# Optimization experiments

Hardware: AMD Instinct MI355X
Metric: run time of the kernel (lower is better)

Reference implementation:

```python
import jax, jax.numpy as jnp
import numpy as np

N = 4096     # nagents
OBS = 256    # obs_size
HID = 256    # hid_size
G = 64       # gat_hid_size
H1 = 4       # gat_num_heads (so H1*G == HID)
H2 = 1       # gat_num_heads_out
A = 64       # actions
QMAX = 255.0  # 2**quant_bits - 1, quant_min = 0
NEG_SLOPE = 0.2


def _lstm_cell(x, h, c, Wih, Whh, bih, bhh):
    gates = x @ Wih.T + bih + h @ Whh.T + bhh
    i, f, g, o = jnp.split(gates, 4, axis=-1)
    c2 = jax.nn.sigmoid(f) * c + jax.nn.sigmoid(i) * jnp.tanh(g)
    h2 = jax.nn.sigmoid(o) * jnp.tanh(c2)
    return h2, c2


def _gat(x, adj, W, a_i, a_j, b, average, self_loop_type):
    # x: [n, in], adj: [n, n], W: [in, H*g], a_i/a_j: [H, g], b: [H*g] or [g_out]
    n = x.shape[0]
    H, g = a_i.shape
    eye = jnp.eye(n, dtype=adj.dtype)
    if self_loop_type == 1:      # force self-loops
        adj = adj * (1.0 - eye) + eye
    elif self_loop_type == 2:    # remove self-loops
        adj = adj * (1.0 - eye)
    h = (x @ W).reshape(n, H, g)                      # [n, H, g]
    ci = jnp.einsum('nhg,hg->hn', h, a_i)             # [H, n]
    cj = jnp.einsum('nhg,hg->hn', h, a_j)             # [H, n]
    e = jax.nn.leaky_relu(ci[:, :, None] + cj[:, None, :], NEG_SLOPE)  # [H, n, n]
    att = jax.nn.softmax(jnp.where(adj[None] > 0, e, -9e15), axis=-1) * adj[None]
    out = jnp.einsum('hij,jhg->ihg', att, h)          # [n, H, g]
    out = out.mean(axis=1) if average else out.reshape(n, H * g)
    return out + b


def _fake_quant(t, bmask):
    # dynamic-range fake quantization over masked entries (min/max detached)
    big = jnp.asarray(1e30, t.dtype)
    mn = jax.lax.stop_gradient(jnp.min(jnp.where(bmask, t, big)))
    mx = jax.lax.stop_gradient(jnp.max(jnp.where(bmask, t, -big)))
    eq = mn == mx
    mn = jnp.where(eq, mn - 0.01, mn)
    mx = jnp.where(eq, mx + 0.01, mx)
    scale = (mx - mn) / QMAX
    zp = jnp.round(-mn / scale)  # quant_min = 0
    deq = (jnp.clip(jnp.round(t / scale + zp), 0.0, QMAX) - zp) * scale
    return jnp.where(bmask, deq, t)


def _qloss(t, bmask):
    return jnp.sum(jnp.where(bmask, jnp.log2(2.0 * QMAX * jnp.abs(t) + 1.0), 0.0))


def _forward(obs, h0, c0, Wobs, bobs, Wih, Whh, bih, bhh,
             W1, ai1, aj1, b1, W2, ai2, aj2, b2, Wv, bv, Wa, ba):
    n = N
    mask = jnp.ones((n, 1), obs.dtype)        # all agents alive
    enc = obs.reshape(n, -1) @ Wobs + bobs    # obs encoder, squeeze batch=1
    h, c = _lstm_cell(enc, h0, c0, Wih, Whh, bih, bhh)
    comm = h
    bmask = jnp.broadcast_to(mask > 0, comm.shape)
    comm = _fake_quant(comm, bmask)
    loss = _qloss(comm, bmask)
    comm = comm * mask
    adj = jnp.ones((n, n), obs.dtype) * mask * mask.T   # complete graph
    comm = _gat(comm, adj, W1, ai1, aj1, b1, average=False, self_loop_type=1)
    comm = jax.nn.elu(comm)
    bmask2 = jnp.broadcast_to(mask > 0, comm.shape)
    comm = _fake_quant(comm, bmask2)
    loss = loss + _qloss(comm, bmask2)
    comm = _gat(comm, adj, W2, ai2, aj2, b2, average=True, self_loop_type=1)
    comm = comm * mask
    value = jnp.concatenate([h, comm], axis=-1) @ Wv + bv              # [n, 1]
    feat = jnp.concatenate([h.reshape(1, n, -1), comm.reshape(1, n, -1)], axis=-1)
    logp = jax.nn.log_softmax(feat @ Wa + ba, axis=-1)                 # [1, n, A]
    return logp, value, h, c, loss


def setup_inputs() -> dict:
    key = jax.random.key(0)
    ks = jax.random.split(key, 21)
    def rn(k, shape, sc=0.05):
        return jax.random.normal(k, shape, dtype=jnp.float32) * sc
    return {
        'obs': rn(ks[0], (1, N, OBS), 1.0),
        'h0': rn(ks[1], (N, HID), 1.0),
        'c0': rn(ks[2], (N, HID), 1.0),
        'Wobs': rn(ks[3], (OBS, HID)),
        'bobs': rn(ks[4], (HID,)),
        'Wih': rn(ks[5], (4 * HID, HID)),
        'Whh': rn(ks[6], (4 * HID, HID)),
        'bih': rn(ks[7], (4 * HID,)),
        'bhh': rn(ks[8], (4 * HID,)),
        'W1': rn(ks[9], (HID, H1 * G)),
        'ai1': rn(ks[10], (H1, G)),
        'aj1': rn(ks[11], (H1, G)),
        'b1': rn(ks[12], (H1 * G,)),
        'W2': rn(ks[13], (H1 * G, H2 * HID)),
        'ai2': rn(ks[14], (H2, HID)),
        'aj2': rn(ks[15], (H2, HID)),
        'b2': rn(ks[16], (HID,)),
        'Wv': rn(ks[17], (2 * HID, 1)),
        'bv': rn(ks[18], (1,)),
        'Wa': rn(ks[19], (2 * HID, A)),
        'ba': rn(ks[20], (A,)),
    }


def reference(obs, h0, c0, Wobs, bobs, Wih, Whh, bih, bhh,
              W1, ai1, aj1, b1, W2, ai2, aj2, b2, Wv, bv, Wa, ba):
    return _forward(obs, h0, c0, Wobs, bobs, Wih, Whh, bih, bhh,
                    W1, ai1, aj1, b1, W2, ai2, aj2, b2, Wv, bv, Wa, ba)
```

## Files before the change

### kernel.cpp

```cpp
#include <hip/hip_runtime.h>
#include <math.h>

typedef __attribute__((ext_vector_type(8))) short short8;
typedef __attribute__((ext_vector_type(4))) float floatx4;

__device__ __forceinline__ ushort f2b(float f) {
  unsigned u = __float_as_uint(f);
  unsigned r = u + 0x7FFFu + ((u >> 16) & 1u);
  return (ushort)(r >> 16);
}

__global__ __launch_bounds__(256) void prep_kernel(
    const float* __restrict__ obs, ushort* __restrict__ obs_bf,
    const float* __restrict__ h0, ushort* __restrict__ h0_bf,
    const float* __restrict__ Wih, ushort* __restrict__ Wih_bf,
    const float* __restrict__ Whh, ushort* __restrict__ Whh_bf,
    const float* __restrict__ Wobs, ushort* __restrict__ WobsT,
    const float* __restrict__ W1, ushort* __restrict__ W1T,
    const float* __restrict__ W2, ushort* __restrict__ W2T,
    const float* __restrict__ Wa, const float* __restrict__ Wv,
    const float* __restrict__ ba, const float* __restrict__ bv,
    const float* __restrict__ bih, const float* __restrict__ bhh,
    ushort* __restrict__ WaTe, float* __restrict__ bias_ext, float* __restrict__ bias12)
{
  __shared__ float tile[32][33];
  const int bid = blockIdx.x;
  const int tid = threadIdx.x;
  if (bid < 1024) {
    const int q0 = 262144, q1 = 262144, q2 = 65536, q3 = 65536;
    const int tot = q0 + q1 + q2 + q3;
    for (int idx = bid * 256 + tid; idx < tot; idx += 1024 * 256) {
      const float* s; ushort* d; int i = idx;
      if (i < q0) { s = obs; d = obs_bf; }
      else if ((i -= q0) < q1) { s = h0; d = h0_bf; }
      else if ((i -= q1) < q2) { s = Wih; d = Wih_bf; }
      else { i -= q2; s = Whh; d = Whh_bf; }
      const float4 v = *(const float4*)(s + (size_t)i * 4);
      ushort4 o; o.x = f2b(v.x); o.y = f2b(v.y); o.z = f2b(v.z); o.w = f2b(v.w);
      *(ushort4*)(d + (size_t)i * 4) = o;
    }
  } else if (bid < 1216) {
    const int t = bid - 1024;
    const int mat = t >> 6, sub = t & 63;
    const float* in = mat == 0 ? Wobs : (mat == 1 ? W1 : W2);
    ushort* outp = mat == 0 ? WobsT : (mat == 1 ? W1T : W2T);
    const int c0 = (sub & 7) * 32, r0 = (sub >> 3) * 32;
    const int tx = tid & 31, ty = tid >> 5;
    #pragma unroll
    for (int p = 0; p < 32; p += 8)
      tile[ty + p][tx] = in[(size_t)(r0 + ty + p) * 256 + c0 + tx];
    __syncthreads();
    #pragma unroll
    for (int p = 0; p < 32; p += 8)
      outp[(size_t)(c0 + ty + p) * 256 + r0 + tx] = f2b(tile[tx][ty + p]);
  } else {
    const int idx = (bid - 1216) * 256 + tid;
    if (idx < 65536) {
      const int n = idx >> 9, k = idx & 511;
      const float v = n < 64 ? Wa[(size_t)k * 64 + n] : (n == 64 ? Wv[k] : 0.0f);
      WaTe[idx] = f2b(v);
    } else if (idx < 65536 + 128) {
      const int n = idx - 65536;
      bias_ext[n] = n < 64 ? ba[n] : (n == 64 ? bv[0] : 0.0f);
    } else if (idx < 65536 + 128 + 1024) {
      const int n = idx - 65536 - 128;
      bias12[n] = bih[n] + bhh[n];
    }
  }
}

template<int BM, int BN, bool OUT_BF16>
__global__ __launch_bounds__(256) void mfma_gemm(
    const ushort* __restrict__ A1, int lda1,
    const ushort* __restrict__ B1, int ldb1, int K1,
    const ushort* __restrict__ A2, int lda2,
    const ushort* __restrict__ B2, int ldb2, int K2,
    const float* __restrict__ bias,
    void* __restrict__ Cv, int N)
{
  constexpr int LDT = 40;
  __shared__ __align__(16) ushort As[BM * LDT];
  __shared__ __align__(16) ushort Bs[BN * LDT];
  const int tid = threadIdx.x;
  const int wave = tid >> 6, lane = tid & 63;
  const int wr = wave >> 1, wc = wave & 1;
  const int m0 = blockIdx.y * BM, n0 = blockIdx.x * BN;
  constexpr int MI = BM / 32;
  constexpr int NI = BN / 32;
  floatx4 acc[MI][NI] = {};
  const int r = tid >> 2, kq = tid & 3;
  const int lm = lane & 15, lq = lane >> 4;
  const int Ktot = K1 + K2;
  for (int k0 = 0; k0 < Ktot; k0 += 32) {
    const ushort* A; const ushort* B; int lda, ldb, kk;
    if (k0 < K1) { A = A1; B = B1; lda = lda1; ldb = ldb1; kk = k0; }
    else         { A = A2; B = B2; lda = lda2; ldb = ldb2; kk = k0 - K1; }
    #pragma unroll
    for (int p = 0; p < BM / 64; ++p) {
      const int rr = r + p * 64;
      *(float4*)&As[rr * LDT + kq * 8] =
          *(const float4*)&A[(size_t)(m0 + rr) * lda + kk + kq * 8];
    }
    #pragma unroll
    for (int p = 0; p < BN / 64; ++p) {
      const int rr = r + p * 64;
      *(float4*)&Bs[rr * LDT + kq * 8] =
          *(const float4*)&B[(size_t)(n0 + rr) * ldb + kk + kq * 8];
    }
    __syncthreads();
    short8 af[MI], bfr[NI];
    #pragma unroll
    for (int i = 0; i < MI; ++i)
      af[i] = *(const short8*)&As[(wr * (BM / 2) + i * 16 + lm) * LDT + lq * 8];
    #pragma unroll
    for (int j = 0; j < NI; ++j)
      bfr[j] = *(const short8*)&Bs[(wc * (BN / 2) + j * 16 + lm) * LDT + lq * 8];
    #pragma unroll
    for (int i = 0; i < MI; ++i)
      #pragma unroll
      for (int j = 0; j < NI; ++j)
        acc[i][j] = __builtin_amdgcn_mfma_f32_16x16x32_bf16(af[i], bfr[j], acc[i][j], 0, 0, 0);
    __syncthreads();
  }
  #pragma unroll
  for (int i = 0; i < MI; ++i) {
    #pragma unroll
    for (int j = 0; j < NI; ++j) {
      const int col = n0 + wc * (BN / 2) + j * 16 + lm;
      const float badd = bias ? bias[col] : 0.0f;
      #pragma unroll
      for (int t = 0; t < 4; ++t) {
        const int row = m0 + wr * (BM / 2) + i * 16 + lq * 4 + t;
        const float v = acc[i][j][t] + badd;
        if (OUT_BF16) ((ushort*)Cv)[(size_t)row * N + col] = f2b(v);
        else          ((float*)Cv)[(size_t)row * N + col] = v;
      }
    }
  }
}

__global__ __launch_bounds__(256) void lstm_elem_kernel(
    const float* __restrict__ gates, const float* __restrict__ c0,
    float* __restrict__ h_out, float* __restrict__ c_out, ushort* __restrict__ h_bf,
    float* __restrict__ pmn, float* __restrict__ pmx)
{
  const int i = blockIdx.x, d = threadIdx.x;
  const float* g = gates + (size_t)i * 1024;
  const float xi = g[d], xf = g[256 + d], xg = g[512 + d], xo = g[768 + d];
  const float c = c0[(size_t)i * 256 + d];
  const float si = 1.0f / (1.0f + expf(-xi));
  const float sf = 1.0f / (1.0f + expf(-xf));
  const float so = 1.0f / (1.0f + expf(-xo));
  const float c2 = sf * c + si * tanhf(xg);
  const float h2 = so * tanhf(c2);
  h_out[(size_t)i * 256 + d] = h2;
  c_out[(size_t)i * 256 + d] = c2;
  h_bf[(size_t)i * 256 + d] = f2b(h2);
  float mn = h2, mx = h2;
  #pragma unroll
  for (int o = 32; o > 0; o >>= 1) {
    mn = fminf(mn, __shfl_xor(mn, o));
    mx = fmaxf(mx, __shfl_xor(mx, o));
  }
  __shared__ float smn[4], smx[4];
  if ((d & 63) == 0) { smn[d >> 6] = mn; smx[d >> 6] = mx; }
  __syncthreads();
  if (d == 0) {
    pmn[i] = fminf(fminf(smn[0], smn[1]), fminf(smn[2], smn[3]));
    pmx[i] = fmaxf(fmaxf(smx[0], smx[1]), fmaxf(smx[2], smx[3]));
  }
}

__global__ __launch_bounds__(256) void quant_kernel(
    const float4* __restrict__ x, ushort* __restrict__ q, int n4,
    const float* __restrict__ pmn, const float* __restrict__ pmx, int np,
    float* __restrict__ part)
{
  __shared__ float smn[4], smx[4], sl[4], bmn, bmx;
  float mn = 3.0e38f, mx = -3.0e38f;
  for (int i = threadIdx.x; i < np; i += 256) {
    mn = fminf(mn, pmn[i]); mx = fmaxf(mx, pmx[i]);
  }
  #pragma unroll
  for (int o = 32; o > 0; o >>= 1) {
    mn = fminf(mn, __shfl_xor(mn, o));
    mx = fmaxf(mx, __shfl_xor(mx, o));
  }
  if ((threadIdx.x & 63) == 0) { smn[threadIdx.x >> 6] = mn; smx[threadIdx.x >> 6] = mx; }
  __syncthreads();
  if (threadIdx.x == 0) {
    bmn = fminf(fminf(smn[0], smn[1]), fminf(smn[2], smn[3]));
    bmx = fmaxf(fmaxf(smx[0], smx[1]), fmaxf(smx[2], smx[3]));
  }
  __syncthreads();
  mn = bmn; mx = bmx;
  if (mn == mx) { mn -= 0.01f; mx += 0.01f; }
  const float scale = (mx - mn) / 255.0f;
  const float zp = rintf(-mn / scale);
  float lsum = 0.0f;
  for (int idx = blockIdx.x * 256 + threadIdx.x; idx < n4; idx += gridDim.x * 256) {
    const float4 t = x[idx];
    float d0, d1, d2, d3;
    { float qq = fminf(fmaxf(rintf(t.x / scale + zp), 0.0f), 255.0f);
      d0 = (qq - zp) * scale; lsum += log2f(510.0f * fabsf(d0) + 1.0f); }
    { float qq = fminf(fmaxf(rintf(t.y / scale + zp), 0.0f), 255.0f);
      d1 = (qq - zp) * scale; lsum += log2f(510.0f * fabsf(d1) + 1.0f); }
    { float qq = fminf(fmaxf(rintf(t.z / scale + zp), 0.0f), 255.0f);
      d2 = (qq - zp) * scale; lsum += log2f(510.0f * fabsf(d2) + 1.0f); }
    { float qq = fminf(fmaxf(rintf(t.w / scale + zp), 0.0f), 255.0f);
      d3 = (qq - zp) * scale; lsum += log2f(510.0f * fabsf(d3) + 1.0f); }
    ushort4 o; o.x = f2b(d0); o.y = f2b(d1); o.z = f2b(d2); o.w = f2b(d3);
    *(ushort4*)(q + (size_t)idx * 4) = o;
  }
  #pragma unroll
  for (int o = 32; o > 0; o >>= 1) lsum += __shfl_xor(lsum, o);
  if ((threadIdx.x & 63) == 0) sl[threadIdx.x >> 6] = lsum;
  __syncthreads();
  if (threadIdx.x == 0) part[blockIdx.x] = sl[0] + sl[1] + sl[2] + sl[3];
}

__global__ __launch_bounds__(256) void cicj1_kernel(
    const float* __restrict__ h1, const float* __restrict__ ai, const float* __restrict__ aj,
    float* __restrict__ ci, float* __restrict__ cj)
{
  const int w = threadIdx.x >> 6, lane = threadIdx.x & 63;
  const int i = blockIdx.x * 4 + w;
  #pragma unroll
  for (int hd = 0; hd < 4; ++hd) {
    const float v = h1[(size_t)i * 256 + hd * 64 + lane];
    float pi = v * ai[hd * 64 + lane];
    float pj = v * aj[hd * 64 + lane];
    #pragma unroll
    for (int o = 32; o > 0; o >>= 1) { pi += __shfl_xor(pi, o); pj += __shfl_xor(pj, o); }
    if (lane == 0) { ci[hd * 4096 + i] = pi; cj[hd * 4096 + i] = pj; }
  }
}

__global__ __launch_bounds__(256) void cicj2_kernel(
    const float* __restrict__ h2, const float* __restrict__ ai, const float* __restrict__ aj,
    float* __restrict__ ci, float* __restrict__ cj)
{
  const int w = threadIdx.x >> 6, lane = threadIdx.x & 63;
  const int i = blockIdx.x * 4 + w;
  float pi = 0.f, pj = 0.f;
  #pragma unroll
  for (int r = 0; r < 4; ++r) {
    const float v = h2[(size_t)i * 256 + r * 64 + lane];
    pi += v * ai[r * 64 + lane];
    pj += v * aj[r * 64 + lane];
  }
  #pragma unroll
  for (int o = 32; o > 0; o >>= 1) { pi += __shfl_xor(pi, o); pj += __shfl_xor(pj, o); }
  if (lane == 0) { ci[i] = pi; cj[i] = pj; }
}

__global__ __launch_bounds__(1024) void rank_sort_kernel(
    const float* __restrict__ c, float* __restrict__ sc, int* __restrict__ pm)
{
  __shared__ float lc[4096];
  __shared__ int scnt[16][64];
  const int head = blockIdx.x >> 6;
  const int seg = blockIdx.x & 63;
  const float* ch = c + head * 4096;
  for (int idx = threadIdx.x; idx < 4096; idx += 1024) lc[idx] = ch[idx];
  __syncthreads();
  const int jl = threadIdx.x & 63;
  const int kg = threadIdx.x >> 6;
  const int j = seg * 64 + jl;
  const float my = lc[j];
  int cnt = 0;
  const int k0 = kg * 256;
  #pragma unroll 8
  for (int k = k0; k < k0 + 256; ++k) {
    const float ck = lc[k];
    cnt += (ck < my || (ck == my && k < j)) ? 1 : 0;
  }
  scnt[kg][jl] = cnt;
  __syncthreads();
  if (threadIdx.x < 64) {
    int rank = 0;
    #pragma unroll
    for (int g = 0; g < 16; ++g) rank += scnt[g][threadIdx.x];
    const int jj = seg * 64 + threadIdx.x;
    sc[head * 4096 + rank] = lc[jj];
    pm[head * 4096 + rank] = jj;
  }
}

__global__ __launch_bounds__(128) void local_scan1(
    const float* __restrict__ h1, const float* __restrict__ sc, const int* __restrict__ pm,
    float* __restrict__ PUl, float* __restrict__ PVl,
    float* __restrict__ dUl, float* __restrict__ dVl,
    float* __restrict__ cku, float* __restrict__ ckv,
    float* __restrict__ ckus, float* __restrict__ ckvs)
{
  const int head = blockIdx.x >> 6;
  const int chunk = blockIdx.x & 63;
  const int wave = threadIdx.x >> 6;
  const int lane = threadIdx.x & 63;
  const float cmax = sc[head * 4096 + 4095];
  const int base = head * 4096 + chunk * 64;
  const float cv = sc[base + lane];
  const float u = expf(cv - cmax);
  const float v = expf(0.2f * (cv - cmax));
  const int myj = pm[base + lane];
  const float* hrow = h1 + head * 64 + lane;
  if (wave == 0) {
    float iu = u, iv = v;
    #pragma unroll
    for (int o = 1; o < 64; o <<= 1) {
      const float tu = __shfl_up(iu, o), tv = __shfl_up(iv, o);
      if (lane >= o) { iu += tu; iv += tv; }
    }
    const float totU = __shfl(iu, 63), totV = __shfl(iv, 63);
    dVl[base + lane] = iv - v;
    dUl[base + lane] = totU - (iu - u);
    if (lane == 0) { ckus[head * 64 + chunk] = totU; ckvs[head * 64 + chunk] = totV; }
    float accV = 0.f;
    #pragma unroll 16
    for (int k = 0; k < 64; ++k) {
      const float vk = __shfl(v, k);
      const int j = __shfl(myj, k);
      PVl[(size_t)(base + k) * 64 + lane] = accV;
      accV += vk * hrow[(size_t)j * 256];
    }
    ckv[(head * 64 + chunk) * 64 + lane] = accV;
  } else {
    float accU = 0.f;
    #pragma unroll 16
    for (int k = 63; k >= 0; --k) {
      const float uk = __shfl(u, k);
      const int j = __shfl(myj, k);
      accU += uk * hrow[(size_t)j * 256];
      PUl[(size_t)(base + k) * 64 + lane] = accU;
    }
    cku[(head * 64 + chunk) * 64 + lane] = accU;
  }
}

__global__ __launch_bounds__(256) void local_scan2(
    const float* __restrict__ h2, const float* __restrict__ sc, const int* __restrict__ pm,
    float* __restrict__ PUl, float* __restrict__ PVl,
    float* __restrict__ dUl, float* __restrict__ dVl,
    float* __restrict__ cku, float* __restrict__ ckv,
    float* __restrict__ ckus, float* __restrict__ ckvs)
{
  __shared__ float su[64], sv[64];
  __shared__ int sj[64];
  const int chunk = blockIdx.y;
  const int colgrp = blockIdx.x;
  const int tid = threadIdx.x;
  const int wave = tid >> 6, lane = tid & 63;
  const float cmax = sc[4095];
  const int base = chunk * 64;
  if (tid < 64) {
    const float cv = sc[base + tid];
    const float u = expf(cv - cmax);
    const float v = expf(0.2f * (cv - cmax));
    su[tid] = u; sv[tid] = v; sj[tid] = pm[base + tid];
    if (colgrp == 0) {
      float iu = u, iv = v;
      #pragma unroll
      for (int o = 1; o < 64; o <<= 1) {
        const float tu = __shfl_up(iu, o), tv = __shfl_up(iv, o);
        if (lane >= o) { iu += tu; iv += tv; }
      }
      const float totU = __shfl(iu, 63), totV = __shfl(iv, 63);
      dVl[base + lane] = iv - v;
      dUl[base + lane] = totU - (iu - u);
      if (lane == 0) { ckus[chunk] = totU; ckvs[chunk] = totV; }
    }
  }
  __syncthreads();
  const int col = colgrp * 128 + (wave & 1) * 64 + lane;
  if (wave < 2) {
    float accV = 0.f;
    #pragma unroll 16
    for (int k = 0; k < 64; ++k) {
      PVl[(size_t)(base + k) * 256 + col] = accV;
      accV += sv[k] * h2[(size_t)sj[k] * 256 + col];
    }
    ckv[chunk * 256 + col] = accV;
  } else {
    float accU = 0.f;
    #pragma unroll 16
    for (int k = 63; k >= 0; --k) {
      accU += su[k] * h2[(size_t)sj[k] * 256 + col];
      PUl[(size_t)(base + k) * 256 + col] = accU;
    }
    cku[chunk * 256 + col] = accU;
  }
}

__global__ __launch_bounds__(64) void prefix1_kernel(
    const float* __restrict__ cku, const float* __restrict__ ckv,
    const float* __restrict__ ckus, const float* __restrict__ ckvs,
    float* __restrict__ sufU, float* __restrict__ prefV,
    float* __restrict__ sufUs, float* __restrict__ prefVs)
{
  const int head = blockIdx.x, lane = threadIdx.x;
  float acc = 0.f;
  for (int c = 0; c < 64; ++c) {
    prefV[(head * 65 + c) * 64 + lane] = acc;
    acc += ckv[(head * 64 + c) * 64 + lane];
  }
  prefV[(head * 65 + 64) * 64 + lane] = acc;
  acc = 0.f;
  sufU[(head * 65 + 64) * 64 + lane] = 0.f;
  for (int c = 63; c >= 0; --c) {
    acc += cku[(head * 64 + c) * 64 + lane];
    sufU[(head * 65 + c) * 64 + lane] = acc;
  }
  {
    const float vs = ckvs[head * 64 + lane];
    const float us = ckus[head * 64 + lane];
    float iv = vs, iu = us;
    #pragma unroll
    for (int o = 1; o < 64; o <<= 1) {
      const float tv = __shfl_up(iv, o), tu = __shfl_up(iu, o);
      if (lane >= o) { iv += tv; iu += tu; }
    }
    prefVs[head * 65 + lane] = iv - vs;
    const float totU = __shfl(iu, 63);
    sufUs[head * 65 + lane] = totU - iu + us;
    if (lane == 63) {
      prefVs[head * 65 + 64] = iv;
      sufUs[head * 65 + 64] = 0.f;
    }
  }
}

__global__ __launch_bounds__(256) void prefix2_kernel(
    const float* __restrict__ cku, const float* __restrict__ ckv,
    const float* __restrict__ ckus, const float* __restrict__ ckvs,
    float* __restrict__ sufU, float* __restrict__ prefV,
    float* __restrict__ sufUs, float* __restrict__ prefVs)
{
  const int col = threadIdx.x;
  const int lane = col & 63;
  float acc = 0.f;
  for (int c = 0; c < 64; ++c) {
    prefV[c * 256 + col] = acc;
    acc += ckv[c * 256 + col];
  }
  prefV[64 * 256 + col] = acc;
  acc = 0.f;
  sufU[64 * 256 + col] = 0.f;
  for (int c = 63; c >= 0; --c) {
    acc += cku[c * 256 + col];
    sufU[c * 256 + col] = acc;
  }
  if (col < 64) {
    const float vs = ckvs[lane];
    const float us = ckus[lane];
    float iv = vs, iu = us;
    #pragma unroll
    for (int o = 1; o < 64; o <<= 1) {
      const float tv = __shfl_up(iv, o), tu = __shfl_up(iu, o);
      if (lane >= o) { iv += tv; iu += tu; }
    }
    prefVs[lane] = iv - vs;
    const float totU = __shfl(iu, 63);
    sufUs[lane] = totU - iu + us;
    if (lane == 63) { prefVs[64] = iv; sufUs[64] = 0.f; }
  }
}

__global__ __launch_bounds__(256) void combine1_kernel(
    const float* __restrict__ ci, const float* __restrict__ sc,
    const float* __restrict__ sufU, const float* __restrict__ prefV,
    const float* __restrict__ sufUs, const float* __restrict__ prefVs,
    const float* __restrict__ PUl, const float* __restrict__ PVl,
    const float* __restrict__ dUl, const float* __restrict__ dVl,
    const float* __restrict__ b1, float* __restrict__ out,
    float* __restrict__ pmn, float* __restrict__ pmx)
{
  const int i = blockIdx.x;
  const int head = threadIdx.x >> 6;
  const int lane = threadIdx.x & 63;
  const float* sch = sc + head * 4096;
  const float civ = ci[head * 4096 + i];
  const float cmax = sch[4095];
  const float sarg = civ + cmax;
  const float m = sarg > 0.f ? sarg : 0.2f * sarg;
  const float Af = expf(sarg - m);
  const float Bf = expf(0.2f * sarg - m);
  const float t = -civ;
  int lo = 0, hi = 4096;
  while (lo < hi) {
    const int mid = (lo + hi) >> 1;
    if (sch[mid] > t) hi = mid; else lo = mid + 1;
  }
  const int s = lo;
  float accP, accN, dP, dN;
  if (s == 4096) {
    accP = 0.f; dP = 0.f;
    accN = prefV[(head * 65 + 64) * 64 + lane];
    dN = prefVs[head * 65 + 64];
  } else {
    const int cs = s >> 6;
    accP = sufU[(head * 65 + cs + 1) * 64 + lane] + PUl[(size_t)(head * 4096 + s) * 64 + lane];
    accN = prefV[(head * 65 + cs) * 64 + lane] + PVl[(size_t)(head * 4096 + s) * 64 + lane];
    dP = sufUs[head * 65 + cs + 1] + dUl[head * 4096 + s];
    dN = prefVs[head * 65 + cs] + dVl[head * 4096 + s];
  }
  const float num = Af * accP + Bf * accN;
  const float den = Af * dP + Bf * dN;
  const float o = num / den + b1[head * 64 + lane];
  const float oe = o > 0.f ? o : expm1f(o);
  out[(size_t)i * 256 + head * 64 + lane] = oe;
  float mn = oe, mx = oe;
  #pragma unroll
  for (int of = 32; of > 0; of >>= 1) {
    mn = fminf(mn, __shfl_xor(mn, of));
    mx = fmaxf(mx, __shfl_xor(mx, of));
  }
  __shared__ float smn[4], smx[4];
  if (lane == 0) { smn[head] = mn; smx[head] = mx; }
  __syncthreads();
  if (threadIdx.x == 0) {
    pmn[i] = fminf(fminf(smn[0], smn[1]), fminf(smn[2], smn[3]));
    pmx[i] = fmaxf(fmaxf(smx[0], smx[1]), fmaxf(smx[2], smx[3]));
  }
}

__global__ __launch_bounds__(256) void combine2_kernel(
    const float* __restrict__ ci, const float* __restrict__ sc,
    const float* __restrict__ sufU, const float* __restrict__ prefV,
    const float* __restrict__ sufUs, const float* __restrict__ prefVs,
    const float* __restrict__ PUl, const float* __restrict__ PVl,
    const float* __restrict__ dUl, const float* __restrict__ dVl,
    const float* __restrict__ b2, ushort* __restrict__ outb)
{
  const int i = blockIdx.x;
  const int col = threadIdx.x;
  const float civ = ci[i];
  const float cmax = sc[4095];
  const float sarg = civ + cmax;
  const float m = sarg > 0.f ? sarg : 0.2f * sarg;
  const float Af = expf(sarg - m);
  const float Bf = expf(0.2f * sarg - m);
  const float t = -civ;
  int lo = 0, hi = 4096;
  while (lo < hi) {
    const int mid = (lo + hi) >> 1;
    if (sc[mid] > t) hi = mid; else lo = mid + 1;
  }
  const int s = lo;
  float accP, accN, dP, dN;
  if (s == 4096) {
    accP = 0.f; dP = 0.f;
    accN = prefV[64 * 256 + col];
    dN = prefVs[64];
  } else {
    const int cs = s >> 6;
    accP = sufU[(cs + 1) * 256 + col] + PUl[(size_t)s * 256 + col];
    accN = prefV[cs * 256 + col] + PVl[(size_t)s * 256 + col];
    dP = sufUs[cs + 1] + dUl[s];
    dN = prefVs[cs] + dVl[s];
  }
  const float num = Af * accP + Bf * accN;
  const float den = Af * dP + Bf * dN;
  outb[(size_t)i * 256 + col] = f2b(num / den + b2[col]);
}

__global__ __launch_bounds__(64) void logsoftmax_kernel(
    const float* __restrict__ logits_ext, float* __restrict__ out,
    float* __restrict__ out_value,
    const float* __restrict__ p1, const float* __restrict__ p2,
    float* __restrict__ out_loss)
{
  const int i = blockIdx.x, lane = threadIdx.x;
  if (i == 4096) {
    float s = 0.f;
    #pragma unroll
    for (int k = 0; k < 4; ++k) s += p1[lane + k * 64] + p2[lane + k * 64];
    #pragma unroll
    for (int o = 32; o > 0; o >>= 1) s += __shfl_xor(s, o);
    if (lane == 0) out_loss[0] = s;
    return;
  }
  const float x = logits_ext[(size_t)i * 128 + lane];
  float mx = x;
  #pragma unroll
  for (int o = 32; o > 0; o >>= 1) mx = fmaxf(mx, __shfl_xor(mx, o));
  float e = expf(x - mx);
  #pragma unroll
  for (int o = 32; o > 0; o >>= 1) e += __shfl_xor(e, o);
  out[(size_t)i * 64 + lane] = x - mx - logf(e);
  if (lane == 0) out_value[i] = logits_ext[(size_t)i * 128 + 64];
}

extern "C" void kernel_launch(void* const* d_in, const int* in_sizes, int n_in,
                              void* d_out, int out_size, void* d_ws, size_t ws_size,
                              hipStream_t stream) {
  const float* obs  = (const float*)d_in[0];
  const float* h0   = (const float*)d_in[1];
  const float* c0   = (const float*)d_in[2];
  const float* Wobs = (const float*)d_in[3];
  const float* bobs = (const float*)d_in[4];
  const float* Wih  = (const float*)d_in[5];
  const float* Whh  = (const float*)d_in[6];
  const float* bih  = (const float*)d_in[7];
  const float* bhh  = (const float*)d_in[8];
  const float* W1   = (const float*)d_in[9];
  const float* ai1  = (const float*)d_in[10];
  const float* aj1  = (const float*)d_in[11];
  const float* b1   = (const float*)d_in[12];
  const float* W2   = (const float*)d_in[13];
  const float* ai2  = (const float*)d_in[14];
  const float* aj2  = (const float*)d_in[15];
  const float* b2   = (const float*)d_in[16];
  const float* Wv   = (const float*)d_in[17];
  const float* bv   = (const float*)d_in[18];
  const float* Wa   = (const float*)d_in[19];
  const float* ba   = (const float*)d_in[20];

  float* out       = (float*)d_out;
  float* out_logp  = out;
  float* out_value = out + 262144;
  float* out_h     = out + 266240;
  float* out_c     = out + 1314816;
  float* out_loss  = out + 2363392;

  char* ws = (char*)d_ws;
  float* part1  = (float*)(ws + 256);
  float* part2  = (float*)(ws + 1280);
  float* pmn    = (float*)(ws + 2304);
  float* pmx    = (float*)(ws + 18688);
  const size_t MB = 1048576;
  const size_t base = 35072;
  ushort* obs_bf  = (ushort*)(ws + base);
  ushort* h0_bf   = (ushort*)(ws + base + 2 * MB);
  ushort* Wih_bf  = (ushort*)(ws + base + 4 * MB);
  ushort* Whh_bf  = (ushort*)(ws + base + 4 * MB + 524288);
  ushort* WobsT   = (ushort*)(ws + base + 5 * MB);
  ushort* W1T     = (ushort*)(ws + base + 5 * MB + 131072);
  ushort* W2T     = (ushort*)(ws + base + 5 * MB + 262144);
  ushort* WaTe    = (ushort*)(ws + base + 5 * MB + 393216);
  float*  bias_ext= (float*) (ws + base + 5 * MB + 524288);
  float*  bias12  = (float*) (ws + base + 5 * MB + 525312);
  ushort* enc_bf  = (ushort*)(ws + base + 6 * MB);
  ushort* h_bf    = (ushort*)(ws + base + 8 * MB);
  ushort* comm_q1 = (ushort*)(ws + base + 10 * MB);
  ushort* comm_q2 = (ushort*)(ws + base + 12 * MB);
  ushort* comm2_bf= (ushort*)(ws + base + 14 * MB);
  float*  gates   = (float*) (ws + base + 16 * MB);
  float*  h1      = gates;
  float*  comm1e  = (float*)((char*)gates + 4 * MB);
  float*  h2b     = (float*)((char*)gates + 8 * MB);
  float*  logits  = (float*)((char*)gates + 12 * MB);
  size_t so = base + 32 * MB;
  auto alloc = [&](size_t bytes) { size_t r = so; so += (bytes + 255) & ~255ull; return (char*)ws + r; };
  float* ci1    = (float*)alloc(4 * 4096 * 4);
  float* cj1    = (float*)alloc(4 * 4096 * 4);
  float* sc1    = (float*)alloc(4 * 4096 * 4);
  int*   pm1    = (int*)  alloc(4 * 4096 * 4);
  float* cku1   = (float*)alloc(4 * 64 * 64 * 4);
  float* ckv1   = (float*)alloc(4 * 64 * 64 * 4);
  float* ckus1  = (float*)alloc(4 * 64 * 4);
  float* ckvs1  = (float*)alloc(4 * 64 * 4);
  float* sufU1  = (float*)alloc(4 * 65 * 64 * 4);
  float* prefV1 = (float*)alloc(4 * 65 * 64 * 4);
  float* sufUs1 = (float*)alloc(4 * 65 * 4);
  float* prefVs1= (float*)alloc(4 * 65 * 4);
  float* ci2    = (float*)alloc(4096 * 4);
  float* cj2    = (float*)alloc(4096 * 4);
  float* sc2    = (float*)alloc(4096 * 4);
  int*   pm2    = (int*)  alloc(4096 * 4);
  float* cku2   = (float*)alloc(64 * 256 * 4);
  float* ckv2   = (float*)alloc(64 * 256 * 4);
  float* ckus2  = (float*)alloc(64 * 4);
  float* ckvs2  = (float*)alloc(64 * 4);
  float* sufU2  = (float*)alloc(65 * 256 * 4);
  float* prefV2 = (float*)alloc(65 * 256 * 4);
  float* sufUs2 = (float*)alloc(65 * 4);
  float* prefVs2= (float*)alloc(65 * 4);
  float* PUl    = (float*)alloc(4 * 4096 * 64 * 4);
  float* PVl    = (float*)alloc(4 * 4096 * 64 * 4);
  float* dUl    = (float*)alloc(4 * 4096 * 4);
  float* dVl    = (float*)alloc(4 * 4096 * 4);

  const dim3 b256(256);
  const int N4 = 262144;

  prep_kernel<<<dim3(1477), b256, 0, stream>>>(
      obs, obs_bf, h0, h0_bf, Wih, Wih_bf, Whh, Whh_bf,
      Wobs, WobsT, W1, W1T, W2, W2T,
      Wa, Wv, ba, bv, bih, bhh, WaTe, bias_ext, bias12);
  mfma_gemm<64, 64, true><<<dim3(4, 64), b256, 0, stream>>>(
      obs_bf, 256, WobsT, 256, 256, nullptr, 0, nullptr, 0, 0, bobs, enc_bf, 256);
  mfma_gemm<128, 128, false><<<dim3(8, 32), b256, 0, stream>>>(
      enc_bf, 256, Wih_bf, 256, 256, h0_bf, 256, Whh_bf, 256, 256, bias12, gates, 1024);
  lstm_elem_kernel<<<dim3(4096), b256, 0, stream>>>(gates, c0, out_h, out_c, h_bf, pmn, pmx);
  quant_kernel<<<dim3(256), b256, 0, stream>>>(
      (const float4*)out_h, comm_q1, N4, pmn, pmx, 4096, part1);
  mfma_gemm<64, 64, false><<<dim3(4, 64), b256, 0, stream>>>(
      comm_q1, 256, W1T, 256, 256, nullptr, 0, nullptr, 0, 0, nullptr, h1, 256);
  cicj1_kernel<<<dim3(1024), b256, 0, stream>>>(h1, ai1, aj1, ci1, cj1);
  rank_sort_kernel<<<dim3(256), dim3(1024), 0, stream>>>(cj1, sc1, pm1);
  local_scan1<<<dim3(256), dim3(128), 0, stream>>>(h1, sc1, pm1,
      PUl, PVl, dUl, dVl, cku1, ckv1, ckus1, ckvs1);
  prefix1_kernel<<<dim3(4), dim3(64), 0, stream>>>(cku1, ckv1, ckus1, ckvs1,
                                                   sufU1, prefV1, sufUs1, prefVs1);
  combine1_kernel<<<dim3(4096), b256, 0, stream>>>(ci1, sc1,
      sufU1, prefV1, sufUs1, prefVs1, PUl, PVl, dUl, dVl, b1, comm1e, pmn, pmx);
  quant_kernel<<<dim3(256), b256, 0, stream>>>(
      (const float4*)comm1e, comm_q2, N4, pmn, pmx, 4096, part2);
  mfma_gemm<64, 64, false><<<dim3(4, 64), b256, 0, stream>>>(
      comm_q2, 256, W2T, 256, 256, nullptr, 0, nullptr, 0, 0, nullptr, h2b, 256);
  cicj2_kernel<<<dim3(1024), b256, 0, stream>>>(h2b, ai2, aj2, ci2, cj2);
  rank_sort_kernel<<<dim3(64), dim3(1024), 0, stream>>>(cj2, sc2, pm2);
  local_scan2<<<dim3(2, 64), b256, 0, stream>>>(h2b, sc2, pm2,
      PUl, PVl, dUl, dVl, cku2, ckv2, ckus2, ckvs2);
  prefix2_kernel<<<dim3(1), b256, 0, stream>>>(cku2, ckv2, ckus2, ckvs2,
                                               sufU2, prefV2, sufUs2, prefVs2);
  combine2_kernel<<<dim3(4096), b256, 0, stream>>>(ci2, sc2,
      sufU2, prefV2, sufUs2, prefVs2, PUl, PVl, dUl, dVl, b2, comm2_bf);
  mfma_gemm<64, 64, false><<<dim3(2, 64), b256, 0, stream>>>(
      h_bf, 256, WaTe, 512, 256, comm2_bf, 256, WaTe + 256, 512, 256,
      bias_ext, logits, 128);
  logsoftmax_kernel<<<dim3(4097), dim3(64), 0, stream>>>(
      logits, out_logp, out_value, part1, part2, out_loss);
}
```

Baseline: 258.3 us.

## Fuse LSTM gate GEMM with cell update and heads GEMM with log-softmax

The Wih/Whh rows and the bias are interleaved during prep so that each 128-column GEMM tile holds complete i/f/g/o groups. The LSTM elementwise update then runs in the GEMM epilogue through shared memory, which removes the 16 MB fp32 gates round-trip and one launch. The actor/value GEMM is likewise fused with log-softmax into one kernel. The rank sort now compares packed 64-bit keys (value bits plus index) in a single compare per element instead of a float compare with a tie-break. In exchange, the fused kernel uses more shared memory, and the partial min/max count drops to 256 per-tile entries.

```diff
diff --git a/kernel.cpp b/kernel.cpp
--- a/kernel.cpp
+++ b/kernel.cpp
@@ -30,14 +30,22 @@
     const int q0 = 262144, q1 = 262144, q2 = 65536, q3 = 65536;
     const int tot = q0 + q1 + q2 + q3;
     for (int idx = bid * 256 + tid; idx < tot; idx += 1024 * 256) {
-      const float* s; ushort* d; int i = idx;
-      if (i < q0) { s = obs; d = obs_bf; }
-      else if ((i -= q0) < q1) { s = h0; d = h0_bf; }
-      else if ((i -= q1) < q2) { s = Wih; d = Wih_bf; }
-      else { i -= q2; s = Whh; d = Whh_bf; }
-      const float4 v = *(const float4*)(s + (size_t)i * 4);
+      const float* s; ushort* d; size_t soff, doff; int i = idx;
+      if (i < q0) { s = obs; d = obs_bf; soff = doff = (size_t)i * 4; }
+      else if ((i -= q0) < q1) { s = h0; d = h0_bf; soff = doff = (size_t)i * 4; }
+      else if ((i -= q1) < q2) {
+        const int pr = i >> 6, k4 = i & 63;
+        const int orow = (pr & 3) * 256 + (pr >> 2);
+        s = Wih; d = Wih_bf; soff = (size_t)orow * 256 + k4 * 4; doff = (size_t)pr * 256 + k4 * 4;
+      } else {
+        i -= q2;
+        const int pr = i >> 6, k4 = i & 63;
+        const int orow = (pr & 3) * 256 + (pr >> 2);
+        s = Whh; d = Whh_bf; soff = (size_t)orow * 256 + k4 * 4; doff = (size_t)pr * 256 + k4 * 4;
+      }
+      const float4 v = *(const float4*)(s + soff);
       ushort4 o; o.x = f2b(v.x); o.y = f2b(v.y); o.z = f2b(v.z); o.w = f2b(v.w);
-      *(ushort4*)(d + (size_t)i * 4) = o;
+      *(ushort4*)(d + doff) = o;
     }
   } else if (bid < 1216) {
     const int t = bid - 1024;
@@ -63,8 +71,9 @@
       const int n = idx - 65536;
       bias_ext[n] = n < 64 ? ba[n] : (n == 64 ? bv[0] : 0.0f);
     } else if (idx < 65536 + 128 + 1024) {
-      const int n = idx - 65536 - 128;
-      bias12[n] = bih[n] + bhh[n];
+      const int pc = idx - 65536 - 128;
+      const int orow = (pc & 3) * 256 + (pc >> 2);
+      bias12[pc] = bih[orow] + bhh[orow];
     }
   }
 }
@@ -139,35 +148,106 @@
   }
 }
 
-__global__ __launch_bounds__(256) void lstm_elem_kernel(
-    const float* __restrict__ gates, const float* __restrict__ c0,
+__global__ __launch_bounds__(256) void gates_lstm_kernel(
+    const ushort* __restrict__ enc_bf, const ushort* __restrict__ Wihp,
+    const ushort* __restrict__ h0_bf, const ushort* __restrict__ Whhp,
+    const float* __restrict__ bias12p, const float* __restrict__ c0,
     float* __restrict__ h_out, float* __restrict__ c_out, ushort* __restrict__ h_bf,
     float* __restrict__ pmn, float* __restrict__ pmx)
 {
-  const int i = blockIdx.x, d = threadIdx.x;
-  const float* g = gates + (size_t)i * 1024;
-  const float xi = g[d], xf = g[256 + d], xg = g[512 + d], xo = g[768 + d];
-  const float c = c0[(size_t)i * 256 + d];
-  const float si = 1.0f / (1.0f + expf(-xi));
-  const float sf = 1.0f / (1.0f + expf(-xf));
-  const float so = 1.0f / (1.0f + expf(-xo));
-  const float c2 = sf * c + si * tanhf(xg);
-  const float h2 = so * tanhf(c2);
-  h_out[(size_t)i * 256 + d] = h2;
-  c_out[(size_t)i * 256 + d] = c2;
-  h_bf[(size_t)i * 256 + d] = f2b(h2);
-  float mn = h2, mx = h2;
+  constexpr int LDT = 40;
+  __shared__ __align__(16) ushort As[128 * LDT];
+  __shared__ __align__(16) ushort Bs[128 * LDT];
+  __shared__ __align__(16) float gbuf[64][132];
+  __shared__ float smn[4], smx[4];
+  const int tid = threadIdx.x;
+  const int wave = tid >> 6, lane = tid & 63;
+  const int wr = wave >> 1, wc = wave & 1;
+  const int m0 = blockIdx.y * 128, n0 = blockIdx.x * 128;
+  floatx4 acc[4][4] = {};
+  const int r = tid >> 2, kq = tid & 3;
+  const int lm = lane & 15, lq = lane >> 4;
+  for (int k0 = 0; k0 < 512; k0 += 32) {
+    const ushort* A; const ushort* B; int kk;
+    if (k0 < 256) { A = enc_bf; B = Wihp; kk = k0; }
+    else          { A = h0_bf;  B = Whhp; kk = k0 - 256; }
+    #pragma unroll
+    for (int p = 0; p < 2; ++p) {
+      const int rr = r + p * 64;
+      *(float4*)&As[rr * LDT + kq * 8] =
+          *(const float4*)&A[(size_t)(m0 + rr) * 256 + kk + kq * 8];
+      *(float4*)&Bs[rr * LDT + kq * 8] =
+          *(const float4*)&B[(size_t)(n0 + rr) * 256 + kk + kq * 8];
+    }
+    __syncthreads();
+    short8 af[4], bfr[4];
+    #pragma unroll
+    for (int i = 0; i < 4; ++i)
+      af[i] = *(const short8*)&As[(wr * 64 + i * 16 + lm) * LDT + lq * 8];
+    #pragma unroll
+    for (int j = 0; j < 4; ++j)
+      bfr[j] = *(const short8*)&Bs[(wc * 64 + j * 16 + lm) * LDT + lq * 8];
+    #pragma unroll
+    for (int i = 0; i < 4; ++i)
+      #pragma unroll
+      for (int j = 0; j < 4; ++j)
+        acc[i][j] = __builtin_amdgcn_mfma_f32_16x16x32_bf16(af[i], bfr[j], acc[i][j], 0, 0, 0);
+    __syncthreads();
+  }
+  float mnl = 3.0e38f, mxl = -3.0e38f;
+  const int rr = tid >> 2;
+  const int dd0 = (tid & 3) * 8;
+  #pragma unroll
+  for (int half = 0; half < 2; ++half) {
+    if (wr == half) {
+      #pragma unroll
+      for (int i = 0; i < 4; ++i)
+        #pragma unroll
+        for (int j = 0; j < 4; ++j) {
+          const int col = wc * 64 + j * 16 + lm;
+          const float badd = bias12p[n0 + col];
+          #pragma unroll
+          for (int t = 0; t < 4; ++t)
+            gbuf[i * 16 + lq * 4 + t][col] = acc[i][j][t] + badd;
+        }
+    }
+    __syncthreads();
+    const int ig = m0 + half * 64 + rr;
+    #pragma unroll
+    for (int eh = 0; eh < 2; ++eh) {
+      const int ddb = dd0 + eh * 4;
+      const size_t off = (size_t)ig * 256 + (n0 >> 2) + ddb;
+      const float4 c4 = *(const float4*)&c0[off];
+      float4 hv, cv; ushort4 hb;
+      #pragma unroll
+      for (int q = 0; q < 4; ++q) {
+        const float4 g4 = *(const float4*)&gbuf[rr][(ddb + q) * 4];
+        const float cc = ((const float*)&c4)[q];
+        const float si = 1.0f / (1.0f + expf(-g4.x));
+        const float sf = 1.0f / (1.0f + expf(-g4.y));
+        const float so = 1.0f / (1.0f + expf(-g4.w));
+        const float c2 = sf * cc + si * tanhf(g4.z);
+        const float h2 = so * tanhf(c2);
+        ((float*)&hv)[q] = h2; ((float*)&cv)[q] = c2; ((ushort*)&hb)[q] = f2b(h2);
+        mnl = fminf(mnl, h2); mxl = fmaxf(mxl, h2);
+      }
+      *(float4*)&h_out[off] = hv;
+      *(float4*)&c_out[off] = cv;
+      *(ushort4*)&h_bf[off] = hb;
+    }
+    __syncthreads();
+  }
   #pragma unroll
   for (int o = 32; o > 0; o >>= 1) {
-    mn = fminf(mn, __shfl_xor(mn, o));
-    mx = fmaxf(mx, __shfl_xor(mx, o));
-  }
-  __shared__ float smn[4], smx[4];
-  if ((d & 63) == 0) { smn[d >> 6] = mn; smx[d >> 6] = mx; }
+    mnl = fminf(mnl, __shfl_xor(mnl, o));
+    mxl = fmaxf(mxl, __shfl_xor(mxl, o));
+  }
+  if (lane == 0) { smn[wave] = mnl; smx[wave] = mxl; }
   __syncthreads();
-  if (d == 0) {
-    pmn[i] = fminf(fminf(smn[0], smn[1]), fminf(smn[2], smn[3]));
-    pmx[i] = fmaxf(fmaxf(smx[0], smx[1]), fmaxf(smx[2], smx[3]));
+  if (tid == 0) {
+    const int bid = blockIdx.y * 8 + blockIdx.x;
+    pmn[bid] = fminf(fminf(smn[0], smn[1]), fminf(smn[2], smn[3]));
+    pmx[bid] = fmaxf(fmaxf(smx[0], smx[1]), fmaxf(smx[2], smx[3]));
   }
 }
 
@@ -257,33 +337,36 @@
 __global__ __launch_bounds__(1024) void rank_sort_kernel(
     const float* __restrict__ c, float* __restrict__ sc, int* __restrict__ pm)
 {
-  __shared__ float lc[4096];
+  __shared__ unsigned long long lk[4096];
   __shared__ int scnt[16][64];
   const int head = blockIdx.x >> 6;
   const int seg = blockIdx.x & 63;
   const float* ch = c + head * 4096;
-  for (int idx = threadIdx.x; idx < 4096; idx += 1024) lc[idx] = ch[idx];
+  for (int idx = threadIdx.x; idx < 4096; idx += 1024) {
+    unsigned u = __float_as_uint(ch[idx]);
+    u = (u & 0x80000000u) ? ~u : (u | 0x80000000u);
+    lk[idx] = ((unsigned long long)u << 12) | (unsigned)idx;
+  }
   __syncthreads();
   const int jl = threadIdx.x & 63;
   const int kg = threadIdx.x >> 6;
-  const int j = seg * 64 + jl;
-  const float my = lc[j];
+  const unsigned long long my = lk[seg * 64 + jl];
   int cnt = 0;
   const int k0 = kg * 256;
   #pragma unroll 8
-  for (int k = k0; k < k0 + 256; ++k) {
-    const float ck = lc[k];
-    cnt += (ck < my || (ck == my && k < j)) ? 1 : 0;
-  }
+  for (int k = k0; k < k0 + 256; ++k)
+    cnt += lk[k] < my ? 1 : 0;
   scnt[kg][jl] = cnt;
   __syncthreads();
   if (threadIdx.x < 64) {
     int rank = 0;
     #pragma unroll
     for (int g = 0; g < 16; ++g) rank += scnt[g][threadIdx.x];
-    const int jj = seg * 64 + threadIdx.x;
-    sc[head * 4096 + rank] = lc[jj];
-    pm[head * 4096 + rank] = jj;
+    const unsigned long long kk = lk[seg * 64 + threadIdx.x];
+    unsigned u = (unsigned)(kk >> 12);
+    const float v = __uint_as_float((u & 0x80000000u) ? (u & 0x7fffffffu) : ~u);
+    sc[head * 4096 + rank] = v;
+    pm[head * 4096 + rank] = (int)(kk & 0xFFFu);
   }
 }
 
@@ -564,31 +647,83 @@
   outb[(size_t)i * 256 + col] = f2b(num / den + b2[col]);
 }
 
-__global__ __launch_bounds__(64) void logsoftmax_kernel(
-    const float* __restrict__ logits_ext, float* __restrict__ out,
-    float* __restrict__ out_value,
+__global__ __launch_bounds__(256) void heads_kernel(
+    const ushort* __restrict__ h_bf, const ushort* __restrict__ comm2_bf,
+    const ushort* __restrict__ WaTe, const float* __restrict__ bias_ext,
+    float* __restrict__ out_logp, float* __restrict__ out_value,
     const float* __restrict__ p1, const float* __restrict__ p2,
     float* __restrict__ out_loss)
 {
-  const int i = blockIdx.x, lane = threadIdx.x;
-  if (i == 4096) {
+  constexpr int LDT = 40;
+  __shared__ __align__(16) ushort As[64 * LDT];
+  __shared__ __align__(16) ushort Bs[128 * LDT];
+  __shared__ float lbuf[64][68];
+  const int tid = threadIdx.x;
+  const int wave = tid >> 6, lane = tid & 63;
+  const int wr = wave >> 1, wc = wave & 1;
+  const int m0 = blockIdx.x * 64;
+  const int lm = lane & 15, lq = lane >> 4;
+  floatx4 acc[2][4] = {};
+  const int r = tid >> 2, kq = tid & 3;
+  for (int k0 = 0; k0 < 512; k0 += 32) {
+    const ushort* Asrc = (k0 < 256) ? h_bf : comm2_bf;
+    const int kk = (k0 < 256) ? k0 : k0 - 256;
+    *(float4*)&As[r * LDT + kq * 8] =
+        *(const float4*)&Asrc[(size_t)(m0 + r) * 256 + kk + kq * 8];
+    #pragma unroll
+    for (int p = 0; p < 2; ++p) {
+      const int rr = r + p * 64;
+      *(float4*)&Bs[rr * LDT + kq * 8] =
+          *(const float4*)&WaTe[(size_t)rr * 512 + k0 + kq * 8];
+    }
+    __syncthreads();
+    short8 af[2], bfr[4];
+    #pragma unroll
+    for (int i = 0; i < 2; ++i)
+      af[i] = *(const short8*)&As[(wr * 32 + i * 16 + lm) * LDT + lq * 8];
+    #pragma unroll
+    for (int j = 0; j < 4; ++j)
+      bfr[j] = *(const short8*)&Bs[(wc * 64 + j * 16 + lm) * LDT + lq * 8];
+    #pragma unroll
+    for (int i = 0; i < 2; ++i)
+      #pragma unroll
+      for (int j = 0; j < 4; ++j)
+        acc[i][j] = __builtin_amdgcn_mfma_f32_16x16x32_bf16(af[i], bfr[j], acc[i][j], 0, 0, 0);
+    __syncthreads();
+  }
+  #pragma unroll
+  for (int i = 0; i < 2; ++i)
+    #pragma unroll
+    for (int j = 0; j < 4; ++j) {
+      const int col = wc * 64 + j * 16 + lm;
+      if (col < 65) {
+        const float badd = bias_ext[col];
+        #pragma unroll
+        for (int t = 0; t < 4; ++t)
+          lbuf[wr * 32 + i * 16 + lq * 4 + t][col] = acc[i][j][t] + badd;
+      }
+    }
+  __syncthreads();
+  for (int rr2 = 0; rr2 < 16; ++rr2) {
+    const int row = wave * 16 + rr2;
+    const float x = lbuf[row][lane];
+    float mx = x;
+    #pragma unroll
+    for (int o = 32; o > 0; o >>= 1) mx = fmaxf(mx, __shfl_xor(mx, o));
+    float e = expf(x - mx);
+    #pragma unroll
+    for (int o = 32; o > 0; o >>= 1) e += __shfl_xor(e, o);
+    out_logp[(size_t)(m0 + row) * 64 + lane] = x - mx - logf(e);
+    if (lane == 0) out_value[m0 + row] = lbuf[row][64];
+  }
+  if (blockIdx.x == 0 && wave == 0) {
     float s = 0.f;
     #pragma unroll
     for (int k = 0; k < 4; ++k) s += p1[lane + k * 64] + p2[lane + k * 64];
     #pragma unroll
     for (int o = 32; o > 0; o >>= 1) s += __shfl_xor(s, o);
     if (lane == 0) out_loss[0] = s;
-    return;
-  }
-  const float x = logits_ext[(size_t)i * 128 + lane];
-  float mx = x;
-  #pragma unroll
-  for (int o = 32; o > 0; o >>= 1) mx = fmaxf(mx, __shfl_xor(mx, o));
-  float e = expf(x - mx);
-  #pragma unroll
-  for (int o = 32; o > 0; o >>= 1) e += __shfl_xor(e, o);
-  out[(size_t)i * 64 + lane] = x - mx - logf(e);
-  if (lane == 0) out_value[i] = logits_ext[(size_t)i * 128 + 64];
+  }
 }
 
 extern "C" void kernel_launch(void* const* d_in, const int* in_sizes, int n_in,
@@ -645,11 +780,10 @@
   ushort* comm_q1 = (ushort*)(ws + base + 10 * MB);
   ushort* comm_q2 = (ushort*)(ws + base + 12 * MB);
   ushort* comm2_bf= (ushort*)(ws + base + 14 * MB);
-  float*  gates   = (float*) (ws + base + 16 * MB);
-  float*  h1      = gates;
-  float*  comm1e  = (float*)((char*)gates + 4 * MB);
-  float*  h2b     = (float*)((char*)gates + 8 * MB);
-  float*  logits  = (float*)((char*)gates + 12 * MB);
+  float*  scratch = (float*) (ws + base + 16 * MB);
+  float*  h1      = scratch;
+  float*  comm1e  = (float*)((char*)scratch + 4 * MB);
+  float*  h2b     = (float*)((char*)scratch + 8 * MB);
   size_t so = base + 32 * MB;
   auto alloc = [&](size_t bytes) { size_t r = so; so += (bytes + 255) & ~255ull; return (char*)ws + r; };
   float* ci1    = (float*)alloc(4 * 4096 * 4);
@@ -690,11 +824,10 @@
       Wa, Wv, ba, bv, bih, bhh, WaTe, bias_ext, bias12);
   mfma_gemm<64, 64, true><<<dim3(4, 64), b256, 0, stream>>>(
       obs_bf, 256, WobsT, 256, 256, nullptr, 0, nullptr, 0, 0, bobs, enc_bf, 256);
-  mfma_gemm<128, 128, false><<<dim3(8, 32), b256, 0, stream>>>(
-      enc_bf, 256, Wih_bf, 256, 256, h0_bf, 256, Whh_bf, 256, 256, bias12, gates, 1024);
-  lstm_elem_kernel<<<dim3(4096), b256, 0, stream>>>(gates, c0, out_h, out_c, h_bf, pmn, pmx);
+  gates_lstm_kernel<<<dim3(8, 32), b256, 0, stream>>>(
+      enc_bf, Wih_bf, h0_bf, Whh_bf, bias12, c0, out_h, out_c, h_bf, pmn, pmx);
   quant_kernel<<<dim3(256), b256, 0, stream>>>(
-      (const float4*)out_h, comm_q1, N4, pmn, pmx, 4096, part1);
+      (const float4*)out_h, comm_q1, N4, pmn, pmx, 256, part1);
   mfma_gemm<64, 64, false><<<dim3(4, 64), b256, 0, stream>>>(
       comm_q1, 256, W1T, 256, 256, nullptr, 0, nullptr, 0, 0, nullptr, h1, 256);
   cicj1_kernel<<<dim3(1024), b256, 0, stream>>>(h1, ai1, aj1, ci1, cj1);
@@ -717,9 +850,6 @@
                                                sufU2, prefV2, sufUs2, prefVs2);
   combine2_kernel<<<dim3(4096), b256, 0, stream>>>(ci2, sc2,
       sufU2, prefV2, sufUs2, prefVs2, PUl, PVl, dUl, dVl, b2, comm2_bf);
-  mfma_gemm<64, 64, false><<<dim3(2, 64), b256, 0, stream>>>(
-      h_bf, 256, WaTe, 512, 256, comm2_bf, 256, WaTe + 256, 512, 256,
-      bias_ext, logits, 128);
-  logsoftmax_kernel<<<dim3(4097), dim3(64), 0, stream>>>(
-      logits, out_logp, out_value, part1, part2, out_loss);
-}
+  heads_kernel<<<dim3(64), b256, 0, stream>>>(
+      h_bf, comm2_bf, WaTe, bias_ext, out_logp, out_value, part1, part2, out_loss);
+}
```

Result: faster. 245.6 us (-4.9%).
